# Kernel tuning notes

Measured on AMD Instinct MI355X. Metric: run time of the kernel, lower is better.

Reference implementation:

```python
import jax, jax.numpy as jnp
import numpy as np

P = 7          # corr_size (patch size)
PAD = P // 2   # displacement radius
PP = P * P     # 49 correlation channels
CHANS = [512, 1024, 512, 256, 256, 256]
HW = [64, 32, 16, 8, 4, 2]
B = 8


def _spatial_correlation(f1, f2):
    """out[b, pi*P+pj, y, x] = sum_c f1[b,c,y,x] * f2[b,c,y+pi-PAD, x+pj-PAD] (zero pad)."""
    Bb, C, H, W = f1.shape
    f2p = jnp.pad(f2, ((0, 0), (0, 0), (PAD, PAD), (PAD, PAD)))
    outs = [jnp.sum(f1 * f2p[:, :, di:di + H, dj:dj + W], axis=1)
            for di in range(P) for dj in range(P)]
    return jnp.stack(outs, axis=1)  # [B, P*P, H, W]


def _corr_lstm_cell(feat, feat_pre, h_pre, c_pre, w, b):
    corr = jax.nn.leaky_relu(_spatial_correlation(feat, feat_pre), 0.01)  # [B,49,H,W]
    lstm_in = jnp.concatenate([corr, h_pre], axis=1)                      # [B,98,H,W]
    conv = jax.lax.conv_general_dilated(
        lstm_in, w, window_strides=(1, 1), padding='SAME',
        dimension_numbers=('NCHW', 'OIHW', 'NCHW')) + b[None, :, None, None]
    cc_i, cc_f, cc_o, cc_g = jnp.split(conv, 4, axis=1)
    i = jax.nn.sigmoid(cc_i)
    f = jax.nn.sigmoid(cc_f)
    o = jax.nn.sigmoid(cc_o)
    g = jnp.tanh(cc_g)
    c_next = f * c_pre + i * g
    h_next = o * jnp.tanh(c_next)
    return h_next, c_next, corr


def setup_inputs() -> dict:
    key = jax.random.key(0)
    ks = jax.random.split(key, 6 * 6)
    d = {}
    ki = 0
    for l in range(6):
        C, S = CHANS[l], HW[l]
        d[f'x{l}'] = 0.05 * jax.random.normal(ks[ki], (B, C, S, S), jnp.float32); ki += 1
        d[f'xp{l}'] = 0.05 * jax.random.normal(ks[ki], (B, C, S, S), jnp.float32); ki += 1
        d[f'h{l}'] = 0.1 * jax.random.normal(ks[ki], (B, PP, S, S), jnp.float32); ki += 1
        d[f'c{l}'] = 0.1 * jax.random.normal(ks[ki], (B, PP, S, S), jnp.float32); ki += 1
        fan_in = 2 * PP * 9
        lim = float(np.sqrt(6.0 / (fan_in + 4 * PP * 9)))
        d[f'w{l}'] = jax.random.uniform(ks[ki], (4 * PP, 2 * PP, 3, 3), jnp.float32, -lim, lim); ki += 1
        bias = jnp.zeros((4 * PP,), jnp.float32).at[PP:2 * PP].set(1.0)  # forget-gate bias = 1
        d[f'b{l}'] = bias; ki += 1
    return d


def reference(x0, x1, x2, x3, x4, x5,
              xp0, xp1, xp2, xp3, xp4, xp5,
              h0, h1, h2, h3, h4, h5,
              c0, c1, c2, c3, c4, c5,
              w0, w1, w2, w3, w4, w5,
              b0, b1, b2, b3, b4, b5):
    xs = [x0, x1, x2, x3, x4, x5]
    xps = [xp0, xp1, xp2, xp3, xp4, xp5]
    hs = [h0, h1, h2, h3, h4, h5]
    cs = [c0, c1, c2, c3, c4, c5]
    ws = [w0, w1, w2, w3, w4, w5]
    bs = [b0, b1, b2, b3, b4, b5]
    outs = []
    for l in range(6):
        outs.append(_corr_lstm_cell(xs[l], xps[l], hs[l], cs[l], ws[l], bs[l]))
    h_next = tuple(o[0] for o in outs)
    c_next = tuple(o[1] for o in outs)
    corrs = tuple(o[2] for o in outs)
    return h_next + c_next + corrs  # flat 18-tuple
```

## Files before the change

kernel.cpp:

```cpp
#include <hip/hip_runtime.h>
#include <stdint.h>

#define DEV __device__ __forceinline__

typedef _Float16 half2_t __attribute__((ext_vector_type(2)));
typedef _Float16 half4_t __attribute__((ext_vector_type(4)));
typedef __bf16   bf16x8  __attribute__((ext_vector_type(8)));
typedef float    floatx4 __attribute__((ext_vector_type(4)));
typedef float    floatx2 __attribute__((ext_vector_type(2)));

DEV float fdot2f(half2_t a, half2_t b, float c) {
#if __has_builtin(__builtin_amdgcn_fdot2)
  return __builtin_amdgcn_fdot2(a, b, c, false);
#else
  return c + (float)a[0] * (float)b[0] + (float)a[1] * (float)b[1];
#endif
}

DEV half2_t pkh2(float a, float b) {
#if __has_builtin(__builtin_amdgcn_cvt_pkrtz)
  return __builtin_bit_cast(half2_t, __builtin_amdgcn_cvt_pkrtz(a, b));
#else
  half2_t r; r[0] = (_Float16)a; r[1] = (_Float16)b; return r;
#endif
}

DEV uint32_t f2bf(float f) {
  uint32_t u = __float_as_uint(f);
  return (u + 0x7FFFu + ((u >> 16) & 1u)) >> 16;
}

DEV void tile_barrier() {
  __builtin_amdgcn_sched_barrier(0);
  asm volatile("s_waitcnt lgkmcnt(0)" ::: "memory");
  __builtin_amdgcn_s_barrier();
  __builtin_amdgcn_sched_barrier(0);
}

struct CorrCfg {
  const float* gx[6]; const float* gxp[6];
  int wg_start[2];
  int mid_start;
  int small_start[3];
  int S[2], C[2], tiles_x[2], tiles_pb[2], cpl[2];
  int mcpl;
  int sS[3], sC[3], sNspl[3];
  long long poff[2], mpoff, spoff[3];
};

__global__ __launch_bounds__(256)
void corr_kernel(CorrCfg cfg, _Float16* __restrict__ partial)
{
  __shared__ half2_t ldsbuf[2][2][22*40] __attribute__((aligned(16)));
  const int tid = threadIdx.x;
  int wg = blockIdx.x;

  if (wg >= cfg.small_start[0]) {
    int lvl = (wg >= cfg.small_start[2]) ? 2 : (wg >= cfg.small_start[1]) ? 1 : 0;
    long long i = (long long)(wg - cfg.small_start[lvl])*256 + tid;
    const int S = cfg.sS[lvl], C = cfg.sC[lvl], SS = S*S;
    const int nsp = cfg.sNspl[lvl];
    const long long per = (long long)8*49*SS;
    if (i >= (long long)nsp*per) return;
    int sp = (int)(i / per);
    long long rem = i - (long long)sp*per;
    const int cpl = C / nsp, cbase = sp * cpl;
    const float* X  = cfg.gx[lvl+3];
    const float* XP = cfg.gxp[lvl+3];
    int xc_ = (int)(rem % S); int yc = (int)((rem/S) % S);
    int d = (int)((rem/SS) % 49); int b = (int)(rem/((long long)49*SS));
    int yy = yc + d/7 - 3, xx = xc_ + (d%7) - 3;
    float s = 0.f;
    if (yy >= 0 && yy < S && xx >= 0 && xx < S) {
      const float* xb = X  + ((size_t)b*C + cbase)*SS + (size_t)yc*S + xc_;
      const float* pb = XP + ((size_t)b*C + cbase)*SS + (size_t)yy*S + xx;
      #pragma unroll 8
      for (int c = 0; c < cpl; ++c) s += xb[(size_t)c*SS] * pb[(size_t)c*SS];
    }
    partial[cfg.spoff[lvl] + (long long)sp*per + rem] = (_Float16)s;
    return;
  }

  if (wg >= cfg.mid_start) {
    constexpr int NT = 256, MS = 16, MC = 512;
    constexpr int ROWS = 22, COLS = 22, ST = 23;
    constexpr int SLOTS = ROWS * 6 * 2;
    constexpr int PER = 2;
    int rel = wg - cfg.mid_start;
    const int cpl = cfg.mcpl;
    const int sp = rel >> 3;
    const int b = rel & 7;
    const int tx = tid & 15, ty = tid >> 4;
    const int cbase = sp * cpl;
    const size_t SS = (size_t)MS*MS;
    const float* Xb  = cfg.gx[2]  + (size_t)b*MC*SS;
    const float* XPb = cfg.gxp[2] + (size_t)b*MC*SS;
    const size_t qoff = (size_t)ty*MS + tx;

    int f_go[PER], f_base[PER], f_col0[PER], f_pr[PER];
    bool f_ok[PER], f_val[PER];
    #pragma unroll
    for (int s = 0; s < PER; ++s) {
      int i = tid + s*NT;
      bool val = (i < SLOTS);
      int ii = val ? i : 0;
      int pr = ii & 1;
      int rest = ii >> 1;
      int q = rest % 6;
      int r = rest / 6;
      int gy = r - 3;
      int gx0 = -4 + 4*q;
      bool ok = val && gy >= 0 && gy < MS && gx0 >= 0 && (gx0 + 3) < MS;
      f_val[s] = val; f_ok[s] = ok; f_pr[s] = pr;
      f_go[s] = ok ? gy*MS + gx0 : 0;
      f_col0[s] = 4*q - 1;
      f_base[s] = r*ST;
    }

    float acc[49];
    #pragma unroll
    for (int d = 0; d < 49; ++d) acc[d] = 0.f;
    half2_t pk[PER][4];
    half2_t xq0[2], xq1[2];

#define MFILL_LOADPK(c0v) { \
  _Pragma("unroll") for (int s = 0; s < PER; ++s) { \
    const float* p_ = XPb + (size_t)(cbase + (c0v) + 2*f_pr[s])*SS + f_go[s]; \
    floatx4 a_ = (floatx4)0.f, b2_ = (floatx4)0.f; \
    if (f_ok[s]) { a_ = *(const floatx4*)p_; b2_ = *(const floatx4*)(p_ + SS); } \
    _Pragma("unroll") for (int j = 0; j < 4; ++j) \
      pk[s][j] = pkh2(a_[j], b2_[j]); } }

#define MXLOADPK(dst, c0v) { \
  float t0_ = Xb[(size_t)(cbase + (c0v) + 0)*SS + qoff]; \
  float t1_ = Xb[(size_t)(cbase + (c0v) + 1)*SS + qoff]; \
  float t2_ = Xb[(size_t)(cbase + (c0v) + 2)*SS + qoff]; \
  float t3_ = Xb[(size_t)(cbase + (c0v) + 3)*SS + qoff]; \
  dst[0] = pkh2(t0_, t1_); dst[1] = pkh2(t2_, t3_); }

#define MFILL_STORE(bbv) { \
  _Pragma("unroll") for (int s = 0; s < PER; ++s) if (f_val[s]) { \
    half2_t* plane_ = &ldsbuf[bbv][f_pr[s]][0]; \
    _Pragma("unroll") for (int j = 0; j < 4; ++j) { \
      int col_ = f_col0[s] + j; \
      if (col_ >= 0 && col_ < COLS) \
        plane_[f_base[s] + col_] = pk[s][j]; } } }

#define MCOMPUTE(bbv, xq) { \
  _Pragma("unroll") for (int pr = 0; pr < 2; ++pr) { \
    half2_t xv = xq[pr]; \
    _Pragma("unroll") for (int di = 0; di < 7; ++di) { \
      const half2_t* row_ = &ldsbuf[bbv][pr][(ty+di)*ST + tx]; \
      _Pragma("unroll") for (int dj = 0; dj < 7; ++dj) \
        acc[di*7+dj] = fdot2f(xv, row_[dj], acc[di*7+dj]); } } }

    const int nchunk = cpl >> 2;
    MFILL_LOADPK(0); MXLOADPK(xq0, 0);
    MFILL_STORE(0);
    MFILL_LOADPK(4); MXLOADPK(xq1, 4);
    tile_barrier();
    for (int k = 0; k < nchunk; k += 2) {
      {
        if (k+1 < nchunk) MFILL_STORE(1);
        if (k+2 < nchunk) MFILL_LOADPK((k+2)*4);
        MCOMPUTE(0, xq0);
        if (k+2 < nchunk) MXLOADPK(xq0, (k+2)*4);
        tile_barrier();
      }
      if (k+1 < nchunk) {
        if (k+2 < nchunk) MFILL_STORE(0);
        if (k+3 < nchunk) MFILL_LOADPK((k+3)*4);
        MCOMPUTE(1, xq1);
        if (k+3 < nchunk) MXLOADPK(xq1, (k+3)*4);
        tile_barrier();
      }
    }
#undef MFILL_LOADPK
#undef MXLOADPK
#undef MFILL_STORE
#undef MCOMPUTE

    _Float16* P = partial + cfg.mpoff + ((size_t)sp*8 + b)*49*SS + qoff;
    #pragma unroll
    for (int d = 0; d < 49; ++d) P[(size_t)d*SS] = (_Float16)acc[d];
    return;
  }

  {
    constexpr int NT = 256, TH = 16, TW = 32;
    constexpr int ROWS = TH + 6;
    constexpr int COLS = TW + 6;
    constexpr int QUADS = 10;
    constexpr int ST = TW + 8;
    constexpr int SLOTS = ROWS * QUADS * 2;
    constexpr int PER = 2;

    int lvl = (wg >= cfg.wg_start[1]) ? 1 : 0;
    wg -= cfg.wg_start[lvl];
    const float* X  = cfg.gx[lvl];
    const float* XP = cfg.gxp[lvl];
    const int S = cfg.S[lvl], C = cfg.C[lvl];
    const int txc = cfg.tiles_x[lvl], tpb = cfg.tiles_pb[lvl], cpl = cfg.cpl[lvl];
    const int per_split = 8 * tpb;
    const int sp = wg / per_split;
    const int rem = wg - sp*per_split;
    const int b = rem / tpb;
    const int t = rem - b*tpb;
    const int y0 = (t / txc) * TH, x0t = (t % txc) * TW;
    const int tx = tid & 15, ty = tid >> 4;
    const int cbase = sp * cpl;
    const size_t SS = (size_t)S*S;
    const float* Xb  = X  + (size_t)b*C*SS;
    const float* XPb = XP + (size_t)b*C*SS;
    const int py = y0 + ty, px = x0t + 2*tx;
    const size_t qoff = (size_t)py*S + px;

    int f_go[PER], f_base[PER], f_col0[PER], f_pr[PER];
    bool f_ok[PER], f_val[PER];
    #pragma unroll
    for (int s = 0; s < PER; ++s) {
      int i = tid + s*NT;
      bool val = (i < SLOTS);
      int ii = val ? i : 0;
      int pr = ii & 1;
      int rest = ii >> 1;
      int q = rest % QUADS;
      int r = rest / QUADS;
      int gy = y0 + r - 3;
      int gx0 = x0t - 4 + 4*q;
      bool ok = val && gy >= 0 && gy < S && gx0 >= 0 && (gx0 + 3) < S;
      f_val[s] = val; f_ok[s] = ok; f_pr[s] = pr;
      f_go[s] = ok ? gy*S + gx0 : 0;
      f_col0[s] = 4*q - 1;
      f_base[s] = r*ST;
    }

    floatx2 acc[49];
    #pragma unroll
    for (int d = 0; d < 49; ++d) acc[d] = (floatx2)0.f;
    half2_t pk[PER][4];
    half2_t xq0[4], xq1[4];

#define FILL_LOADPK(c0v) { \
  _Pragma("unroll") for (int s = 0; s < PER; ++s) { \
    const float* p_ = XPb + (size_t)(cbase + (c0v) + 2*f_pr[s])*SS + f_go[s]; \
    floatx4 a_ = (floatx4)0.f, b2_ = (floatx4)0.f; \
    if (f_ok[s]) { a_ = *(const floatx4*)p_; b2_ = *(const floatx4*)(p_ + SS); } \
    _Pragma("unroll") for (int j = 0; j < 4; ++j) \
      pk[s][j] = pkh2(a_[j], b2_[j]); } }

#define XLOADPK(dst, c0v) { \
  floatx2 t0_ = *(const floatx2*)(Xb + (size_t)(cbase + (c0v) + 0)*SS + qoff); \
  floatx2 t1_ = *(const floatx2*)(Xb + (size_t)(cbase + (c0v) + 1)*SS + qoff); \
  floatx2 t2_ = *(const floatx2*)(Xb + (size_t)(cbase + (c0v) + 2)*SS + qoff); \
  floatx2 t3_ = *(const floatx2*)(Xb + (size_t)(cbase + (c0v) + 3)*SS + qoff); \
  dst[0] = pkh2(t0_.x, t1_.x); dst[1] = pkh2(t0_.y, t1_.y); \
  dst[2] = pkh2(t2_.x, t3_.x); dst[3] = pkh2(t2_.y, t3_.y); }

#define FILL_STORE(bbv) { \
  _Pragma("unroll") for (int s = 0; s < PER; ++s) if (f_val[s]) { \
    half2_t* plane_ = &ldsbuf[bbv][f_pr[s]][0]; \
    _Pragma("unroll") for (int j = 0; j < 4; ++j) { \
      int col_ = f_col0[s] + j; \
      if (col_ >= 0 && col_ < COLS) \
        plane_[f_base[s] + col_] = pk[s][j]; } } }

#define COMPUTE(bbv, xq) { \
  _Pragma("unroll") for (int pr = 0; pr < 2; ++pr) { \
    half2_t xqa = xq[2*pr], xqb = xq[2*pr+1]; \
    _Pragma("unroll") for (int di = 0; di < 7; ++di) { \
      const half2_t* row_ = &ldsbuf[bbv][pr][(ty+di)*ST + 2*tx]; \
      half2_t L_[8]; \
      _Pragma("unroll") for (int k = 0; k < 4; ++k) { \
        half4_t v_ = *(const half4_t*)(row_ + 2*k); \
        L_[2*k]   = __builtin_shufflevector(v_, v_, 0, 1); \
        L_[2*k+1] = __builtin_shufflevector(v_, v_, 2, 3); } \
      _Pragma("unroll") for (int dj = 0; dj < 7; ++dj) { \
        acc[di*7+dj].x = fdot2f(xqa, L_[dj],   acc[di*7+dj].x); \
        acc[di*7+dj].y = fdot2f(xqb, L_[dj+1], acc[di*7+dj].y); } } } }

    const int nchunk = cpl >> 2;
    FILL_LOADPK(0); XLOADPK(xq0, 0);
    FILL_STORE(0);
    FILL_LOADPK(4); XLOADPK(xq1, 4);
    tile_barrier();
    for (int k = 0; k < nchunk; k += 2) {
      {
        if (k+1 < nchunk) FILL_STORE(1);
        if (k+2 < nchunk) FILL_LOADPK((k+2)*4);
        COMPUTE(0, xq0);
        if (k+2 < nchunk) XLOADPK(xq0, (k+2)*4);
        tile_barrier();
      }
      if (k+1 < nchunk) {
        if (k+2 < nchunk) FILL_STORE(0);
        if (k+3 < nchunk) FILL_LOADPK((k+3)*4);
        COMPUTE(1, xq1);
        if (k+3 < nchunk) XLOADPK(xq1, (k+3)*4);
        tile_barrier();
      }
    }
#undef FILL_LOADPK
#undef XLOADPK
#undef FILL_STORE
#undef COMPUTE

    _Float16* P = partial + cfg.poff[lvl] + ((size_t)sp*8 + b)*49*SS + qoff;
    #pragma unroll
    for (int d = 0; d < 49; ++d) {
      half2_t pko = pkh2(acc[d].x, acc[d].y);
      *(uint32_t*)(P + (size_t)d*SS) = *(const uint32_t*)&pko;
    }
  }
}

__global__ __launch_bounds__(256)
void pack_w_kernel(const float* __restrict__ w0, const float* __restrict__ w1,
                   const float* __restrict__ w2, const float* __restrict__ w3,
                   const float* __restrict__ w4, const float* __restrict__ w5,
                   uint16_t* __restrict__ wpack)
{
  int idx = blockIdx.x*256 + threadIdx.x;
  int lvl = idx / 258048;
  int e = idx - lvl*258048;
  const float* W = lvl==0?w0:lvl==1?w1:lvl==2?w2:lvl==3?w3:lvl==4?w4:w5;
  int j = e & 7, lane = (e >> 3) & 63, rest = e >> 9;
  int s = rest % 36, tt = rest / 36;
  int n  = tt*16 + (lane & 15);
  int ch = (s & 3)*32 + (lane >> 4)*8 + j;
  int tap = s >> 2, ky = tap/3, kx = tap - 3*ky;
  float v = 0.f;
  if (n < 196 && ch < 98) v = W[((n*98 + ch)*3 + ky)*3 + kx];
  wpack[idx] = (uint16_t)f2bf(v);
}

struct P2Cfg {
  int blk_start[7];
  int S[6], nsplit[6], pxg[6], lg[6], gpb[6];
  long long poff[6], lstm_off[6], corr_off[6];
  const float* h[6];
};
__global__ __launch_bounds__(256)
void pass2_kernel(P2Cfg cfg, const _Float16* __restrict__ partial,
                  uint32_t* __restrict__ lstm, float* __restrict__ dout)
{
  __shared__ float lds[64*99];
  int blk = blockIdx.x;
  int lvl = 0;
  while (lvl < 5 && blk >= cfg.blk_start[lvl+1]) ++lvl;
  int rel = blk - cfg.blk_start[lvl];
  const int S = cfg.S[lvl], Sp = S + 2, SS = S*S;
  const int PXG = cfg.pxg[lvl], lg = cfg.lg[lvl], gpb = cfg.gpb[lvl];
  const int b = rel / gpb, g = rel - b*gpb;
  const int pixbase = g * PXG;
  const int tid = threadIdx.x;
  const int nsp = cfg.nsplit[lvl];
  const size_t spstride = (size_t)8*49*SS;
  const int quads = PXG >> 2;
  const int lq = lg - 2;
  for (int e = tid; e < quads*98; e += 256) {
    int qx = e & (quads - 1);
    int ch = e >> lq;
    int pix = pixbase + 4*qx;
    floatx4 v;
    if (ch < 49) {
      const _Float16* P = partial + cfg.poff[lvl] + ((size_t)b*49 + ch)*SS + pix;
      floatx4 s = (floatx4)0.f;
      for (int sp = 0; sp < nsp; ++sp) {
        half4_t pv = *(const half4_t*)(P + (size_t)sp*spstride);
        s[0] += (float)pv[0]; s[1] += (float)pv[1];
        s[2] += (float)pv[2]; s[3] += (float)pv[3];
      }
      #pragma unroll
      for (int j = 0; j < 4; ++j) s[j] = s[j] < 0.f ? 0.01f*s[j] : s[j];
      *(floatx4*)(dout + cfg.corr_off[lvl] + ((size_t)b*49 + ch)*SS + pix) = s;
      v = s;
    } else {
      v = *(const floatx4*)(cfg.h[lvl] + ((size_t)b*49 + (ch - 49))*SS + pix);
    }
    int pxl = 4*qx;
    lds[(pxl+0)*99 + ch] = v[0];
    lds[(pxl+1)*99 + ch] = v[1];
    lds[(pxl+2)*99 + ch] = v[2];
    lds[(pxl+3)*99 + ch] = v[3];
  }
  __syncthreads();
  uint32_t* Lb = lstm + (cfg.lstm_off[lvl] >> 1);
  for (int f = tid; f < (PXG << 6); f += 256) {
    int pxl = f >> 6, c2 = f & 63;
    int pix = pixbase + pxl;
    int y = pix / S, x = pix - y*S;
    int c0 = 2*c2, c1 = c0 + 1;
    float v0 = c0 < 98 ? lds[pxl*99 + c0] : 0.f;
    float v1 = c1 < 98 ? lds[pxl*99 + c1] : 0.f;
    Lb[((size_t)(b*Sp + y + 1)*Sp + (x + 1))*64 + c2] = f2bf(v0) | (f2bf(v1) << 16);
  }
}

struct CCfg {
  int wg_start[7];
  int S[6], tiles_x[6], tiles_pb[6], lwsh[6], mfc[6], mgrp[6];
  long long lstm_off[6], wp_off[6], h_off[6], c_off[6];
  const float* cpre[6]; const float* bias[6];
};
__global__ __launch_bounds__(256)
void conv_kernel(CCfg cfg, const uint16_t* __restrict__ lstm,
                 const uint16_t* __restrict__ wpack, float* __restrict__ dout)
{
  __shared__ float gl[224*69];
  int wg = blockIdx.x;
  int lvl = 0;
  while (lvl < 5 && wg >= cfg.wg_start[lvl+1]) ++lvl;
  wg -= cfg.wg_start[lvl];
  const int S = cfg.S[lvl], Sp = S + 2;
  const int lwsh = cfg.lwsh[lvl], msk = (1 << lwsh) - 1;
  const int tpb = cfg.tiles_pb[lvl];
  const int b = wg / tpb, t = wg - b*tpb;
  const int ty0 = (t / cfg.tiles_x[lvl]) << (6 - lwsh);
  const int tx0 = (t % cfg.tiles_x[lvl]) << lwsh;
  const int tid = threadIdx.x;
  const int wave = tid >> 6, lane = tid & 63;
  const int nhalf = wave & 1, mhalf = wave >> 1;
  const int mfc = cfg.mfc[lvl];
  const bool active = (mhalf < cfg.mgrp[lvl]);
  const int mi = lane & 15, q = lane >> 4;
  const int SS = S*S;

  if (active) {
    const uint16_t* lb = lstm + cfg.lstm_off[lvl] + (size_t)b*Sp*Sp*128;
    int aoff[2];
    #pragma unroll
    for (int mf = 0; mf < 2; ++mf) {
      int p = mhalf*32 + mf*16 + mi;
      int pc = p < SS ? p : 0;
      int y = ty0 + (pc >> lwsh), xx = tx0 + (pc & msk);
      aoff[mf] = (y*Sp + xx)*128 + q*8;
    }
    const uint16_t* wb = wpack + cfg.wp_off[lvl]
                       + (size_t)(nhalf*7)*36*512 + (size_t)lane*8;
    floatx4 acc[2][7];
    #pragma unroll
    for (int mf = 0; mf < 2; ++mf)
      #pragma unroll
      for (int nt = 0; nt < 7; ++nt) acc[mf][nt] = (floatx4)0.0f;

#define CONV_LOAD(sv, AV, BV) { \
  int tap_ = (sv) >> 2, cs_ = (sv) & 3; \
  int ky_ = tap_ / 3, kx_ = tap_ - 3*ky_; \
  int ao_ = ((ky_*Sp + kx_) << 7) + (cs_ << 5); \
  _Pragma("unroll") for (int mf = 0; mf < 2; ++mf) \
    if (mf < mfc) AV[mf] = *(const bf16x8*)(lb + aoff[mf] + ao_); \
  _Pragma("unroll") for (int nt = 0; nt < 7; ++nt) \
    BV[nt] = *(const bf16x8*)(wb + (size_t)((nt)*36 + (sv))*512); }

#define CONV_MFMA(AV, BV) { \
  _Pragma("unroll") for (int nt = 0; nt < 7; ++nt) \
    _Pragma("unroll") for (int mf = 0; mf < 2; ++mf) \
      if (mf < mfc) acc[mf][nt] = __builtin_amdgcn_mfma_f32_16x16x32_bf16( \
                        AV[mf], BV[nt], acc[mf][nt], 0, 0, 0); }

    bf16x8 av0[2], bv0[7], av1[2], bv1[7];
    CONV_LOAD(0, av0, bv0);
    for (int s = 0; s < 36; s += 2) {
      CONV_LOAD(s+1, av1, bv1);
      CONV_MFMA(av0, bv0);
      if (s+2 < 36) CONV_LOAD(s+2, av0, bv0);
      CONV_MFMA(av1, bv1);
    }
#undef CONV_LOAD
#undef CONV_MFMA

    #pragma unroll
    for (int mf = 0; mf < 2; ++mf) {
      if (mf < mfc) {
        #pragma unroll
        for (int nt = 0; nt < 7; ++nt) {
          const int n = nhalf*112 + nt*16 + mi;
          if (n < 196) {
            #pragma unroll
            for (int r = 0; r < 4; ++r) {
              const int p = mhalf*32 + mf*16 + q*4 + r;
              gl[n*69 + p] = acc[mf][nt][r];
            }
          }
        }
      }
    }
  }
  __syncthreads();

  const int p2 = lane;
  const int grp = wave;
  if (p2 < SS) {
    const int y = ty0 + (p2 >> lwsh), xx = tx0 + (p2 & msk);
    const int pix = y*S + xx;
    const float* bb2 = cfg.bias[lvl];
    const float* cp  = cfg.cpre[lvl];
    const int ch0 = grp*13, chend = (grp == 3) ? 49 : grp*13 + 13;
    for (int ch = ch0; ch < chend; ++ch) {
      float ci  = gl[ch*69 + p2]        + bb2[ch];
      float cf  = gl[(ch+49)*69 + p2]   + bb2[ch+49];
      float co_ = gl[(ch+98)*69 + p2]   + bb2[ch+98];
      float cg  = gl[(ch+147)*69 + p2]  + bb2[ch+147];
      float ig = 1.f/(1.f + __expf(-ci));
      float fg = 1.f/(1.f + __expf(-cf));
      float og = 1.f/(1.f + __expf(-co_));
      float g  = 1.f - 2.f/(__expf(2.f*cg) + 1.f);
      size_t e = ((size_t)b*49 + ch)*SS + pix;
      float cpv = cp[e];
      float cn = fg*cpv + ig*g;
      float hn = og * (1.f - 2.f/(__expf(2.f*cn) + 1.f));
      dout[cfg.h_off[lvl] + e] = hn;
      dout[cfg.c_off[lvl] + e] = cn;
    }
  }
}

extern "C" void kernel_launch(void* const* d_in, const int* in_sizes, int n_in,
                              void* d_out, int out_size, void* d_ws, size_t ws_size,
                              hipStream_t stream)
{
  const float *x[6], *xp[6], *h[6], *cpre[6], *w[6], *bias[6];
  for (int l = 0; l < 6; ++l) {
    x[l]    = (const float*)d_in[6*l + 0];
    xp[l]   = (const float*)d_in[6*l + 1];
    h[l]    = (const float*)d_in[6*l + 2];
    cpre[l] = (const float*)d_in[6*l + 3];
    w[l]    = (const float*)d_in[6*l + 4];
    bias[l] = (const float*)d_in[6*l + 5];
  }
  static const int SL[6] = {64,32,16,8,4,2};
  static const int CL[6] = {512,1024,512,256,256,256};
  int NSPL[6] = {8,16,16,1,1,1};

  long long hsz[6], lstm_off[6], h_off[6], poff[6];
  long long a1 = 0, a3 = 0;
  for (int l = 0; l < 6; ++l) {
    int S = SL[l], Sp = S + 2;
    hsz[l] = 8LL*49*S*S;
    lstm_off[l] = a1; a1 += 8LL*Sp*Sp*128;
    h_off[l]    = a3; a3 += hsz[l];
  }
  long long pa = 0;
  for (int l = 0; l < 6; ++l) { poff[l] = pa; pa += (long long)NSPL[l]*hsz[l]; }
  {
    long long need = a1*2 + 6LL*258048*2 + pa*2;
    if (need > (long long)ws_size) {
      NSPL[0] = 4; NSPL[1] = 8; NSPL[2] = 16;
      pa = 0;
      for (int l = 0; l < 6; ++l) { poff[l] = pa; pa += (long long)NSPL[l]*hsz[l]; }
    }
  }
  const long long GRP = a3;
  const long long LSTM_ELEMS = a1;

  uint16_t* lstm  = (uint16_t*)d_ws;
  uint16_t* wpack = (uint16_t*)((char*)d_ws + LSTM_ELEMS*2);
  _Float16* partial = (_Float16*)((char*)d_ws + LSTM_ELEMS*2 + 6LL*258048*2);
  float* dout = (float*)d_out;

  {
    CorrCfg ccfg;
    static const int tpb2[2] = {8, 2};
    static const int txx2[2] = {2, 1};
    for (int l = 0; l < 6; ++l) { ccfg.gx[l] = x[l]; ccfg.gxp[l] = xp[l]; }
    int start = 0;
    for (int l = 0; l < 2; ++l) {
      ccfg.wg_start[l] = start;
      ccfg.S[l] = SL[l]; ccfg.C[l] = CL[l];
      ccfg.tiles_x[l] = txx2[l]; ccfg.tiles_pb[l] = tpb2[l];
      ccfg.cpl[l] = CL[l]/NSPL[l];
      ccfg.poff[l] = poff[l];
      start += NSPL[l]*8*tpb2[l];
    }
    ccfg.mid_start = start;
    ccfg.mcpl = CL[2]/NSPL[2];
    ccfg.mpoff = poff[2];
    start += NSPL[2]*8;
    for (int l = 0; l < 3; ++l) {
      ccfg.small_start[l] = start;
      ccfg.sS[l] = SL[l+3]; ccfg.sC[l] = CL[l+3];
      ccfg.sNspl[l] = NSPL[l+3];
      ccfg.spoff[l] = poff[l+3];
      start += (int)((NSPL[l+3]*hsz[l+3] + 255)/256);
    }
    corr_kernel<<<start, 256, 0, stream>>>(ccfg, partial);
  }
  (void)hipMemsetAsync(lstm, 0, (size_t)LSTM_ELEMS*2, stream);
  pack_w_kernel<<<6048, 256, 0, stream>>>(w[0],w[1],w[2],w[3],w[4],w[5], wpack);
  {
    P2Cfg p2; int start = 0;
    static const int PXGL[6] = {32,64,64,64,16,4};
    static const int LGL[6]  = {5,6,6,6,4,2};
    for (int l = 0; l < 6; ++l) {
      p2.blk_start[l] = start;
      int gpb = (SL[l]*SL[l]) / PXGL[l]; if (gpb < 1) gpb = 1;
      p2.gpb[l] = gpb;
      start += 8 * gpb;
      p2.S[l] = SL[l]; p2.nsplit[l] = NSPL[l];
      p2.pxg[l] = PXGL[l]; p2.lg[l] = LGL[l];
      p2.poff[l] = poff[l]; p2.lstm_off[l] = lstm_off[l];
      p2.corr_off[l] = 2*GRP + h_off[l];
      p2.h[l] = h[l];
    }
    p2.blk_start[6] = start;
    pass2_kernel<<<start, 256, 0, stream>>>(p2, partial, (uint32_t*)lstm, dout);
  }
  {
    CCfg cc;
    static const int ctpb[6] = {64, 16, 4, 1, 1, 1};
    static const int ctx[6]  = {4, 2, 1, 1, 1, 1};
    static const int clw[6]  = {4, 4, 4, 3, 2, 1};
    static const int cmfc[6] = {2, 2, 2, 2, 1, 1};
    static const int cmg[6]  = {2, 2, 2, 2, 1, 1};
    int start = 0;
    for (int l = 0; l < 6; ++l) {
      cc.wg_start[l] = start; start += 8*ctpb[l];
      cc.S[l] = SL[l]; cc.tiles_x[l] = ctx[l]; cc.tiles_pb[l] = ctpb[l];
      cc.lwsh[l] = clw[l]; cc.mfc[l] = cmfc[l]; cc.mgrp[l] = cmg[l];
      cc.lstm_off[l] = lstm_off[l];
      cc.wp_off[l] = 258048LL*l;
      cc.h_off[l] = h_off[l];
      cc.c_off[l] = GRP + h_off[l];
      cc.cpre[l] = cpre[l];
      cc.bias[l] = bias[l];
    }
    cc.wg_start[6] = start;
    conv_kernel<<<start, 256, 0, stream>>>(cc, lstm, wpack, dout);
  }
  (void)in_sizes; (void)n_in; (void)out_size; (void)ws_size;
}
```

Before: 434.6 us.

## Fold lstm memset and weight packing into corr kernel; skip padded N tile

Removes the separate hipMemsetAsync and pack_w_kernel launches by appending extra blocks to the correlation kernel's grid that zero the lstm buffer and pack the conv weights to bf16. This saves two launches and their serialization gaps, and lets the auxiliary work run alongside the correlation blocks. Separately, the conv kernel's second N-half wave now does 6 N-tiles instead of 7, skipping the tile that is entirely padding beyond 196 outputs. The memset path assumes LSTM_ELEMS/8 is a multiple of 256, otherwise the tail is left unzeroed.

```diff
diff --git a/kernel.cpp b/kernel.cpp
--- a/kernel.cpp
+++ b/kernel.cpp
@@ -46,6 +46,10 @@
   int mcpl;
   int sS[3], sC[3], sNspl[3];
   long long poff[2], mpoff, spoff[3];
+  const float* w[6];
+  uint16_t* wpk;
+  uint16_t* lstmz;
+  int aux_start, nmemset_blk;
 };
 
 __global__ __launch_bounds__(256)
@@ -54,6 +58,28 @@
   __shared__ half2_t ldsbuf[2][2][22*40] __attribute__((aligned(16)));
   const int tid = threadIdx.x;
   int wg = blockIdx.x;
+
+  if (wg >= cfg.aux_start) {
+    int aw = wg - cfg.aux_start;
+    if (aw < cfg.nmemset_blk) {
+      floatx4* p = (floatx4*)cfg.lstmz;
+      p[(size_t)aw*256 + tid] = (floatx4)0.f;
+    } else {
+      int idx = (aw - cfg.nmemset_blk)*256 + tid;
+      int lvl = idx / 258048;
+      int e = idx - lvl*258048;
+      const float* W = cfg.w[lvl];
+      int j = e & 7, lane = (e >> 3) & 63, rest = e >> 9;
+      int s = rest % 36, tt = rest / 36;
+      int n  = tt*16 + (lane & 15);
+      int ch = (s & 3)*32 + (lane >> 4)*8 + j;
+      int tap = s >> 2, ky = tap/3, kx = tap - 3*ky;
+      float v = 0.f;
+      if (n < 196 && ch < 98) v = W[((n*98 + ch)*3 + ky)*3 + kx];
+      cfg.wpk[idx] = (uint16_t)f2bf(v);
+    }
+    return;
+  }
 
   if (wg >= cfg.small_start[0]) {
     int lvl = (wg >= cfg.small_start[2]) ? 2 : (wg >= cfg.small_start[1]) ? 1 : 0;
@@ -312,26 +338,6 @@
       *(uint32_t*)(P + (size_t)d*SS) = *(const uint32_t*)&pko;
     }
   }
-}
-
-__global__ __launch_bounds__(256)
-void pack_w_kernel(const float* __restrict__ w0, const float* __restrict__ w1,
-                   const float* __restrict__ w2, const float* __restrict__ w3,
-                   const float* __restrict__ w4, const float* __restrict__ w5,
-                   uint16_t* __restrict__ wpack)
-{
-  int idx = blockIdx.x*256 + threadIdx.x;
-  int lvl = idx / 258048;
-  int e = idx - lvl*258048;
-  const float* W = lvl==0?w0:lvl==1?w1:lvl==2?w2:lvl==3?w3:lvl==4?w4:w5;
-  int j = e & 7, lane = (e >> 3) & 63, rest = e >> 9;
-  int s = rest % 36, tt = rest / 36;
-  int n  = tt*16 + (lane & 15);
-  int ch = (s & 3)*32 + (lane >> 4)*8 + j;
-  int tap = s >> 2, ky = tap/3, kx = tap - 3*ky;
-  float v = 0.f;
-  if (n < 196 && ch < 98) v = W[((n*98 + ch)*3 + ky)*3 + kx];
-  wpack[idx] = (uint16_t)f2bf(v);
 }
 
 struct P2Cfg {
@@ -425,6 +431,7 @@
   const bool active = (mhalf < cfg.mgrp[lvl]);
   const int mi = lane & 15, q = lane >> 4;
   const int SS = S*S;
+  const int ntc = 7 - nhalf;
 
   if (active) {
     const uint16_t* lb = lstm + cfg.lstm_off[lvl] + (size_t)b*Sp*Sp*128;
@@ -451,12 +458,12 @@
   _Pragma("unroll") for (int mf = 0; mf < 2; ++mf) \
     if (mf < mfc) AV[mf] = *(const bf16x8*)(lb + aoff[mf] + ao_); \
   _Pragma("unroll") for (int nt = 0; nt < 7; ++nt) \
-    BV[nt] = *(const bf16x8*)(wb + (size_t)((nt)*36 + (sv))*512); }
+    if (nt < ntc) BV[nt] = *(const bf16x8*)(wb + (size_t)((nt)*36 + (sv))*512); }
 
 #define CONV_MFMA(AV, BV) { \
   _Pragma("unroll") for (int nt = 0; nt < 7; ++nt) \
     _Pragma("unroll") for (int mf = 0; mf < 2; ++mf) \
-      if (mf < mfc) acc[mf][nt] = __builtin_amdgcn_mfma_f32_16x16x32_bf16( \
+      if (nt < ntc && mf < mfc) acc[mf][nt] = __builtin_amdgcn_mfma_f32_16x16x32_bf16( \
                         AV[mf], BV[nt], acc[mf][nt], 0, 0, 0); }
 
     bf16x8 av0[2], bv0[7], av1[2], bv1[7];
@@ -584,10 +591,15 @@
       ccfg.spoff[l] = poff[l+3];
       start += (int)((NSPL[l+3]*hsz[l+3] + 255)/256);
     }
-    corr_kernel<<<start, 256, 0, stream>>>(ccfg, partial);
-  }
-  (void)hipMemsetAsync(lstm, 0, (size_t)LSTM_ELEMS*2, stream);
-  pack_w_kernel<<<6048, 256, 0, stream>>>(w[0],w[1],w[2],w[3],w[4],w[5], wpack);
+    for (int l = 0; l < 6; ++l) ccfg.w[l] = w[l];
+    ccfg.wpk = wpack;
+    ccfg.lstmz = lstm;
+    ccfg.aux_start = start;
+    ccfg.nmemset_blk = (int)(LSTM_ELEMS / 8 / 256);
+    int npack_blk = 6048;
+    int grid = start + ccfg.nmemset_blk + npack_blk;
+    corr_kernel<<<grid, 256, 0, stream>>>(ccfg, partial);
+  }
   {
     P2Cfg p2; int start = 0;
     static const int PXGL[6] = {32,64,64,64,16,4};
```

New measurement: 430.8 us. Within noise of the previous version (-0.9%).
